# Kernel tuning notes

Measured on AMD Instinct MI355X. Metric: run time of the kernel, lower is better.

The kernel has to match this reference:

```python
import jax, jax.numpy as jnp
import numpy as np

N, E, M, NT, RB, SH, NIR, LAT = 10000, 160000, 8, 4, 8, 9, 3, 128
AVG_N = 16.0
LATF = LAT + M * NIR  # 152
COMP2IR = np.array([0, 1, 1, 1, 2, 2, 2, 2, 2])  # irrep id per SH component (0e,1o,2e)
IR1H = jnp.asarray(np.eye(NIR, dtype=np.float32)[COMP2IR])  # [9,3] one-hot comp->irrep


def _silu(x):
    return x * jax.nn.sigmoid(x)


def setup_inputs() -> dict:
    key = jax.random.key(0)
    ks = jax.random.split(key, 16)
    def w(k, shape, fan_in):
        return jax.random.normal(k, shape, jnp.float32) / np.sqrt(fan_in)
    return {
        'edge_attrs': jax.random.normal(ks[0], (E, SH), jnp.float32),
        'edge_embedding': jax.random.normal(ks[1], (E, RB), jnp.float32),
        'node_attrs': jax.random.uniform(ks[2], (N, NT), jnp.float32),
        'edge_lengths': jax.random.uniform(ks[3], (E,), jnp.float32),
        'tb_w0': w(ks[4], (2 * NT + RB, LAT), 2 * NT + RB),
        'tb_w1': w(ks[5], (LAT, LAT), LAT),
        'tb_w2': w(ks[6], (LAT, LAT), LAT),
        'env_mlp_w0': w(ks[7], (LAT, 2 * M * NIR), LAT),
        'env_mlp_w1': w(ks[8], (LAT, M * NIR), LAT),
        'env_linear_w': w(ks[9], (2, NIR, M, M), M),
        'latent_w': w(ks[10], (LATF, LAT), LATF),
        'lat2feat_w': w(ks[11], (2, LATF, NIR * M * M), LATF),
        'lat2featold_w': w(ks[12], (2, LATF, NIR * M * M), LATF),
        'final_w': w(ks[13], (LATF, M), LATF),
        'edge_index': jax.random.randint(ks[14], (2, E), 0, N, jnp.int32),
    }


def reference(edge_attrs, edge_embedding, node_attrs, edge_lengths,
              tb_w0, tb_w1, tb_w2, env_mlp_w0, env_mlp_w1, env_linear_w,
              latent_w, lat2feat_w, lat2featold_w, final_w, edge_index):
    center, neigh = edge_index[0], edge_index[1]
    n_nodes = node_attrs.shape[0]
    c2i = jnp.asarray(COMP2IR)

    # polynomial cutoff, p=6, x = r / r_max
    x = edge_lengths
    p = 6.0
    cut = (1.0 - (p + 1) * (p + 2) / 2 * x**6 + p * (p + 2) * x**7 - p * (p + 1) / 2 * x**8)
    cut = jnp.where(x < 1.0, cut, 0.0)[:, None]

    # two-body latent MLP on [center species, neighbor species, radial basis]
    tb_in = jnp.concatenate([node_attrs[center], node_attrs[neigh], edge_embedding], axis=-1)
    h = _silu(tb_in @ tb_w0)
    h = _silu(h @ tb_w1)
    latents = (h @ tb_w2) * cut  # [E, LAT]

    def weight_edges(wch):  # MakeWeightedChannels: per-irrep channel weights
        return wch[:, :, c2i] * edge_attrs[:, None, :]  # [E, M, 9]

    def env_of(w_cur, layer):  # scatter to node env + env linear
        env = jax.ops.segment_sum(weight_edges(w_cur), center, num_segments=n_nodes) / AVG_N
        Wc = env_linear_w[layer][c2i]  # [9, M, M]
        return jnp.einsum('duv,nvd->nud', Wc, env) / np.sqrt(M)

    def interact(features, env_c):  # scalar-gated equivariant coupling
        return features * env_c[:, :, :1] + env_c * features[:, :, :1]

    def invariants(f):  # per-(channel, irrep) norms
        return jnp.sqrt(jnp.einsum('eud,di->eui', f * f, IR1H) + 1e-8).reshape(f.shape[0], M * NIR)

    def pe_linear(Wflat, f):  # per-edge generated irrep-wise Linear
        W = Wflat.reshape(-1, NIR, M, M)
        return jnp.einsum('eiuv,di,evd->eud', W, IR1H, f) / np.sqrt(M)

    # ---- layer 0 (initial weighter + env weighter) ----
    ew = latents @ env_mlp_w0  # [E, 2*M*NIR]
    w_init = ew[:, :M * NIR].reshape(-1, M, NIR)
    w_cur = ew[:, M * NIR:].reshape(-1, M, NIR)
    features = weight_edges(w_init)  # [E, M, 9]
    env_c = env_of(w_cur, 0)[center]
    new_f = interact(features, env_c)
    lat_full = jnp.concatenate([latents, invariants(new_f)], axis=-1)  # [E, 152]
    features = 0.5 * pe_linear(lat_full @ lat2featold_w[0], features) \
             + 0.5 * pe_linear(lat_full @ lat2feat_w[0], new_f)

    # ---- layer 1 ----
    lat_new = _silu(lat_full @ latent_w) * cut
    latents = 0.5 * latents + 0.5 * lat_new  # latent resnet, sigmoid(0)=0.5
    w_cur = (latents @ env_mlp_w1).reshape(-1, M, NIR)
    env_c = env_of(w_cur, 1)[center]
    new_f = interact(features, env_c)
    lat_full = jnp.concatenate([latents, invariants(new_f)], axis=-1)
    features = 0.5 * pe_linear(lat_full @ lat2featold_w[1], features) \
             + 0.5 * pe_linear(lat_full @ lat2feat_w[1], new_f)

    # ---- final: generated linear to 1x1o per edge (components 1:4) ----
    wfin = lat_full @ final_w  # [E, M]
    return jnp.einsum('em,emd->ed', wfin, features[:, :, 1:4]) / np.sqrt(M)
```

## Files before the change

### kernel.cpp

```cpp
#include <hip/hip_runtime.h>
#include <hip/hip_bf16.h>

#define EE 160000
#define NNODES 10000

using bf16 = __hip_bfloat16;
using bf16x8 = __attribute__((ext_vector_type(8))) short;
using short4v = __attribute__((ext_vector_type(4))) short;
using f32x4  = __attribute__((ext_vector_type(4))) float;

__device__ __forceinline__ float silu_f(float x) { return x / (1.0f + __expf(-x)); }
__device__ __forceinline__ float b2f(bf16 v) { return __bfloat162float(v); }
__device__ __forceinline__ bf16 f2b(float v) { return __float2bfloat16(v); }

__device__ __forceinline__ unsigned bfbits(float v) {
    union { float f; unsigned u; } a; a.f = v;
    return (a.u + 0x7fffu + ((a.u >> 16) & 1u)) >> 16;
}
__device__ __forceinline__ unsigned pack2(float a, float b) {
    return bfbits(a) | (bfbits(b) << 16);
}
__device__ __forceinline__ void unpack2(unsigned u, float& a, float& b) {
    union { unsigned x; float f; } lo, hi;
    lo.x = u << 16; hi.x = u & 0xffff0000u;
    a = lo.f; b = hi.f;
}
__device__ __forceinline__ float bs2f(short s) {
    union { unsigned u; float f; } x; x.u = ((unsigned)(unsigned short)s) << 16;
    return x.f;
}

#define INV_AVGN_SQM 0.02209708691207961f
#define HALF_INV_SQM 0.17677669529663687f
#define INV_SQM      0.35355339059327373f

__global__ void kCnt(const int* __restrict__ eidx, int* __restrict__ deg)
{
    const int e = blockIdx.x * 256 + threadIdx.x;
    atomicAdd(&deg[eidx[e]], 1);
}

__global__ void kScan(const int* __restrict__ deg, int* __restrict__ off)
{
    __shared__ int part[256];
    const int t = threadIdx.x;
    int loc[40];
    int s = 0;
#pragma unroll
    for (int i = 0; i < 40; i++) {
        const int idx = t * 40 + i;
        const int v = (idx < NNODES) ? deg[idx] : 0;
        loc[i] = s;
        s += v;
    }
    part[t] = s;
    __syncthreads();
    for (int d = 1; d < 256; d <<= 1) {
        const int v = (t >= d) ? part[t - d] : 0;
        __syncthreads();
        part[t] += v;
        __syncthreads();
    }
    const int base = (t == 0) ? 0 : part[t - 1];
#pragma unroll
    for (int i = 0; i < 40; i++) {
        const int idx = t * 40 + i;
        if (idx < NNODES) off[idx] = base + loc[i];
    }
    if (t == 255) off[NNODES] = part[255];
}

__global__ void kFill(const int* __restrict__ eidx, int* __restrict__ cur,
                      const int* __restrict__ off, int* __restrict__ elist)
{
    const int e = blockIdx.x * 256 + threadIdx.x;
    const int c = eidx[e];
    const int pos = atomicAdd(&cur[c], 1);
    elist[off[c] + pos] = e;
}

__global__ void kPrepA(const float* __restrict__ w1, const float* __restrict__ w2,
                       const float* __restrict__ wm0, short* __restrict__ wAt)
{
    const int t = blockIdx.x * 256 + threadIdx.x;
    if (t >= 38912) return;
    const int k = t & 127, c = t >> 7;
    float v;
    if (c < 128)      v = w1[k * 128 + c];
    else if (c < 256) v = w2[k * 128 + (c - 128)];
    else              v = wm0[k * 48 + (c - 256)];
    wAt[c * 128 + k] = (short)bfbits(v);
}

__global__ void kPrepB(const float* __restrict__ l2fo, const float* __restrict__ l2fn,
                       const float* __restrict__ latw, const float* __restrict__ l2fo1,
                       const float* __restrict__ l2fn1, const float* __restrict__ finw,
                       const float* __restrict__ wm1, short* __restrict__ Bt)
{
    const int k = blockIdx.y;
    const int col = blockIdx.x * 256 + threadIdx.x;
    if (col >= 672) return;
    float v = 0.f;
    if (col < 648) {
        if (k < 152) {
            if (col < 384) {
                const int ir = col >> 7, half = (col >> 6) & 1, q = col & 63;
                const float* src = half ? l2fn : l2fo;
                v = src[k * 192 + ir * 64 + q];
            } else if (col < 512)  v = latw[k * 128 + (col - 384)];
            else if (col < 576)    v = l2fo1[k * 192 + 64 + (col - 512)];
            else if (col < 640)    v = l2fn1[k * 192 + 64 + (col - 576)];
            else                   v = finw[k * 8 + (col - 640)];
        }
    } else {
        if (k < 128) v = wm1[k * 24 + (col - 648)];
    }
    Bt[(size_t)col * 160 + k] = (short)bfbits(v);
}

__global__ void kEnvG(const float* __restrict__ wcur, const float* __restrict__ ea,
                      const int* __restrict__ off, const int* __restrict__ elist,
                      const float* __restrict__ wl, float* __restrict__ envc)
{
    const int t = blockIdx.x * 256 + threadIdx.x;
    if (t >= NNODES * 9) return;
    const int n = t / 9;
    const int d = t - n * 9;
    const int irr = (d == 0) ? 0 : ((d < 4) ? 1 : 2);
    float v[8];
#pragma unroll
    for (int q = 0; q < 8; q++) v[q] = 0.0f;
    const int b = off[n], en = off[n + 1];
    for (int j = b; j < en; j++) {
        const int e = elist[j];
        const float ad = ea[e * 9 + d];
        const float* wr = wcur + (size_t)e * 24 + irr;
#pragma unroll
        for (int q = 0; q < 8; q++) v[q] = fmaf(wr[q * 3], ad, v[q]);
    }
#pragma unroll
    for (int u = 0; u < 8; u++) {
        float s = 0.0f;
#pragma unroll
        for (int q = 0; q < 8; q++) s = fmaf(wl[irr * 64 + u * 8 + q], v[q], s);
        envc[n * 72 + u * 9 + d] = s * INV_AVGN_SQM;
    }
}

__global__ __launch_bounds__(256) void kA0(
    const float* __restrict__ ea, const float* __restrict__ eemb,
    const float* __restrict__ nat, const float* __restrict__ elen,
    const float* __restrict__ w0, const int* __restrict__ eidx,
    short* __restrict__ h08, short* __restrict__ latf8s,
    bf16* __restrict__ eaT, float* __restrict__ cutb)
{
    __shared__ float w0s[16 * 128];
    const int t = threadIdx.x;
    const int e = blockIdx.x * 256 + t;
#pragma unroll
    for (int p = 0; p < 8; p++) { const int idx = p * 256 + t; w0s[idx] = w0[idx]; }
    __syncthreads();

    const int ctr = eidx[e];
    const int ngb = eidx[EE + e];
    float tin[16];
#pragma unroll
    for (int k = 0; k < 4; k++) tin[k] = nat[ctr * 4 + k];
#pragma unroll
    for (int k = 0; k < 4; k++) tin[4 + k] = nat[ngb * 4 + k];
#pragma unroll
    for (int k = 0; k < 8; k++) tin[8 + k] = eemb[e * 8 + k];

    const float x = elen[e];
    const float x2 = x * x, x4 = x2 * x2, x6 = x4 * x2, x7 = x6 * x, x8 = x7 * x;
    float cutv = 1.0f - 28.0f * x6 + 48.0f * x7 - 21.0f * x8;
    cutv = (x < 1.0f) ? cutv : 0.0f;
    cutb[e] = cutv;

    const size_t tb = (size_t)(e >> 5);
    const int el = e & 31;
#pragma unroll
    for (int jc = 0; jc < 4; jc++) {
        float a[32];
#pragma unroll
        for (int j = 0; j < 32; j++) a[j] = 0.0f;
#pragma unroll
        for (int k = 0; k < 16; k++) {
            const float v = tin[k];
#pragma unroll
            for (int j = 0; j < 32; j++) a[j] = fmaf(v, w0s[k * 128 + jc * 32 + j], a[j]);
        }
#pragma unroll
        for (int cc = 0; cc < 4; cc++) {
            bf16x8 hv;
#pragma unroll
            for (int jj = 0; jj < 8; jj++) hv[jj] = (short)bfbits(silu_f(a[cc * 8 + jj]));
            *(bf16x8*)(h08 + tb * 4096 + (jc * 4 + cc) * 256 + el * 8) = hv;
        }
    }
    bf16x8 z;
#pragma unroll
    for (int jj = 0; jj < 8; jj++) z[jj] = 0;
    *(bf16x8*)(latf8s + tb * 5120 + 19 * 256 + el * 8) = z;

#pragma unroll
    for (int d = 0; d < 9; d++) eaT[(size_t)d * EE + e] = f2b(ea[e * 9 + d]);
}

__global__ __launch_bounds__(256, 2) void kAm(
    const short* __restrict__ h08, const short* __restrict__ wAt,
    const float* __restrict__ cutb, short* __restrict__ latf8s,
    float* __restrict__ winiF, float* __restrict__ wcur0)
{
    __shared__ short Bs[16 * 128 * 8];
    __shared__ alignas(16) char a2raw[16384];
    __shared__ short A3[8192];
    short* A2 = (short*)a2raw;
    float* Cs = (float*)a2raw;

    const int t = threadIdx.x;
    const int eb = blockIdx.x * 64;
    const int lane = t & 63, wid = t >> 6;
    const int wm = wid >> 1, wn = wid & 1;
    const int l15 = lane & 15, kq = lane >> 4;
    const f32x4 zz = {0.f, 0.f, 0.f, 0.f};

#pragma unroll
    for (int p = 0; p < 8; p++) {
        const int task = p * 256 + t;
        const int n = task & 127, kc = task >> 7;
        *(bf16x8*)(Bs + kc * 1024 + n * 8) = *(const bf16x8*)(wAt + n * 128 + kc * 8);
    }
    float cutR[2][4];
#pragma unroll
    for (int mi = 0; mi < 2; mi++)
#pragma unroll
        for (int r = 0; r < 4; r++)
            cutR[mi][r] = cutb[eb + wm * 32 + mi * 16 + kq * 4 + r];
    __syncthreads();

    {
        f32x4 acc[8];
#pragma unroll
        for (int q = 0; q < 8; q++) acc[q] = zz;
        const size_t ab = (size_t)((eb >> 5) + wm) * 4096 + l15 * 8;
#pragma unroll
        for (int ks = 0; ks < 4; ks++) {
            const int kc = ks * 4 + kq;
            const bf16x8 a0 = *(const bf16x8*)(h08 + ab + kc * 256);
            const bf16x8 a1 = *(const bf16x8*)(h08 + ab + kc * 256 + 128);
            const short* bp = Bs + kc * 1024 + (wn * 64 + l15) * 8;
#pragma unroll
            for (int ni = 0; ni < 4; ni++) {
                const bf16x8 b = *(const bf16x8*)(bp + ni * 128);
                acc[ni]     = __builtin_amdgcn_mfma_f32_16x16x32_bf16(a0, b, acc[ni], 0, 0, 0);
                acc[4 + ni] = __builtin_amdgcn_mfma_f32_16x16x32_bf16(a1, b, acc[4 + ni], 0, 0, 0);
            }
        }
#pragma unroll
        for (int mi = 0; mi < 2; mi++)
#pragma unroll
            for (int ni = 0; ni < 4; ni++) {
                const int kcol = wn * 64 + ni * 16 + l15;
                const int eb2 = wm * 32 + mi * 16 + (kq << 2);
#pragma unroll
                for (int r = 0; r < 4; r++)
                    A2[(kcol >> 3) * 512 + (eb2 + r) * 8 + (kcol & 7)] =
                        (short)bfbits(silu_f(acc[mi * 4 + ni][r]));
            }
    }
    __syncthreads();
#pragma unroll
    for (int p = 0; p < 8; p++) {
        const int task = p * 256 + t;
        const int n = task & 127, kc = task >> 7;
        *(bf16x8*)(Bs + kc * 1024 + n * 8) = *(const bf16x8*)(wAt + 16384 + n * 128 + kc * 8);
    }
    __syncthreads();

    {
        f32x4 acc[8];
#pragma unroll
        for (int q = 0; q < 8; q++) acc[q] = zz;
#pragma unroll
        for (int ks = 0; ks < 4; ks++) {
            const int kc = ks * 4 + kq;
            const bf16x8 a0 = *(const bf16x8*)(A2 + kc * 512 + (wm * 32 + l15) * 8);
            const bf16x8 a1 = *(const bf16x8*)(A2 + kc * 512 + (wm * 32 + 16 + l15) * 8);
            const short* bp = Bs + kc * 1024 + (wn * 64 + l15) * 8;
#pragma unroll
            for (int ni = 0; ni < 4; ni++) {
                const bf16x8 b = *(const bf16x8*)(bp + ni * 128);
                acc[ni]     = __builtin_amdgcn_mfma_f32_16x16x32_bf16(a0, b, acc[ni], 0, 0, 0);
                acc[4 + ni] = __builtin_amdgcn_mfma_f32_16x16x32_bf16(a1, b, acc[4 + ni], 0, 0, 0);
            }
        }
#pragma unroll
        for (int mi = 0; mi < 2; mi++)
#pragma unroll
            for (int ni = 0; ni < 4; ni++) {
                const int kcol = wn * 64 + ni * 16 + l15;
                const int eb2 = wm * 32 + mi * 16 + (kq << 2);
#pragma unroll
                for (int r = 0; r < 4; r++)
                    A3[(kcol >> 3) * 512 + (eb2 + r) * 8 + (kcol & 7)] =
                        (short)bfbits(acc[mi * 4 + ni][r] * cutR[mi][r]);
            }
    }
    __syncthreads();
#pragma unroll
    for (int p = 0; p < 8; p++) {
        const int task = p * 256 + t;
        const int n = task & 127, kc = task >> 7;
        bf16x8 bv;
        if (n < 48) bv = *(const bf16x8*)(wAt + 32768 + n * 128 + kc * 8);
        else {
#pragma unroll
            for (int jj = 0; jj < 8; jj++) bv[jj] = 0;
        }
        *(bf16x8*)(Bs + kc * 1024 + n * 8) = bv;
    }
#pragma unroll
    for (int p = 0; p < 4; p++) {
        const int i = p * 256 + t;
        const int e = i & 63, kc = i >> 6;
        const bf16x8 v = *(const bf16x8*)(A3 + kc * 512 + e * 8);
        const int eg = eb + e;
        *(bf16x8*)(latf8s + (size_t)(eg >> 5) * 5120 + kc * 256 + (eg & 31) * 8) = v;
    }
    __syncthreads();

    if (wn == 0) {
        f32x4 acc[6];
#pragma unroll
        for (int q = 0; q < 6; q++) acc[q] = zz;
#pragma unroll
        for (int ks = 0; ks < 4; ks++) {
            const int kc = ks * 4 + kq;
            const bf16x8 a0 = *(const bf16x8*)(A3 + kc * 512 + (wm * 32 + l15) * 8);
            const bf16x8 a1 = *(const bf16x8*)(A3 + kc * 512 + (wm * 32 + 16 + l15) * 8);
            const short* bp = Bs + kc * 1024 + l15 * 8;
#pragma unroll
            for (int ni = 0; ni < 3; ni++) {
                const bf16x8 b = *(const bf16x8*)(bp + ni * 128);
                acc[ni]     = __builtin_amdgcn_mfma_f32_16x16x32_bf16(a0, b, acc[ni], 0, 0, 0);
                acc[3 + ni] = __builtin_amdgcn_mfma_f32_16x16x32_bf16(a1, b, acc[3 + ni], 0, 0, 0);
            }
        }
#pragma unroll
        for (int mi = 0; mi < 2; mi++)
#pragma unroll
            for (int ni = 0; ni < 3; ni++) {
                const int c = ni * 16 + l15;
                const int eb2 = wm * 32 + mi * 16 + (kq << 2);
#pragma unroll
                for (int r = 0; r < 4; r++)
                    Cs[c * 65 + eb2 + r] = acc[mi * 3 + ni][r];
            }
    }
    __syncthreads();
    for (int i = t; i < 1536; i += 256) {
        const int c = i >> 6, e = i & 63;
        winiF[(size_t)c * EE + eb + e] = Cs[c * 65 + e];
    }
    for (int i = t; i < 1536; i += 256) {
        const int e2 = i / 24, c2 = i - e2 * 24;
        wcur0[(size_t)(eb + e2) * 24 + c2] = Cs[(24 + c2) * 65 + e2];
    }
}

__global__ __launch_bounds__(256, 1) void kC1(
    const float* __restrict__ winiF, const bf16* __restrict__ eaT,
    const float* __restrict__ envc, const int* __restrict__ eidx,
    unsigned* __restrict__ newfT, short* __restrict__ latf8s)
{
    const int e = blockIdx.x * 256 + threadIdx.x;
    const int ctr = eidx[e];
    float eav[9];
#pragma unroll
    for (int d = 0; d < 9; d++) eav[d] = b2f(eaT[(size_t)d * EE + e]);
    const float* ec = envc + ctr * 72;
    float inv[24];
#pragma unroll
    for (int uh = 0; uh < 4; uh++) {
        const int u0 = 2 * uh;
        float wi0[3], wi1[3];
#pragma unroll
        for (int i = 0; i < 3; i++) {
            wi0[i] = winiF[(size_t)(u0 * 3 + i) * EE + e];
            wi1[i] = winiF[(size_t)((u0 + 1) * 3 + i) * EE + e];
        }
        float nf0[9], nf1[9];
        const float ec00 = ec[u0 * 9 + 0];
        const float ec10 = ec[(u0 + 1) * 9 + 0];
        const float f00 = wi0[0] * eav[0];
        const float f10 = wi1[0] * eav[0];
#pragma unroll
        for (int d = 0; d < 9; d++) {
            const int irr = (d == 0) ? 0 : ((d < 4) ? 1 : 2);
            const float fa = wi0[irr] * eav[d];
            const float fb = wi1[irr] * eav[d];
            nf0[d] = fa * ec00 + ec[u0 * 9 + d] * f00;
            nf1[d] = fb * ec10 + ec[(u0 + 1) * 9 + d] * f10;
        }
#pragma unroll
        for (int d = 0; d < 9; d++) newfT[(size_t)(d * 4 + uh) * EE + e] = pack2(nf0[d], nf1[d]);
        inv[uh * 6 + 0] = sqrtf(nf0[0] * nf0[0] + 1e-8f);
        inv[uh * 6 + 1] = sqrtf(nf0[1]*nf0[1] + nf0[2]*nf0[2] + nf0[3]*nf0[3] + 1e-8f);
        inv[uh * 6 + 2] = sqrtf(nf0[4]*nf0[4] + nf0[5]*nf0[5] + nf0[6]*nf0[6] + nf0[7]*nf0[7] + nf0[8]*nf0[8] + 1e-8f);
        inv[uh * 6 + 3] = sqrtf(nf1[0] * nf1[0] + 1e-8f);
        inv[uh * 6 + 4] = sqrtf(nf1[1]*nf1[1] + nf1[2]*nf1[2] + nf1[3]*nf1[3] + 1e-8f);
        inv[uh * 6 + 5] = sqrtf(nf1[4]*nf1[4] + nf1[5]*nf1[5] + nf1[6]*nf1[6] + nf1[7]*nf1[7] + nf1[8]*nf1[8] + 1e-8f);
    }
    const size_t tb = (size_t)(e >> 5);
    const int el = e & 31;
#pragma unroll
    for (int j = 0; j < 3; j++) {
        bf16x8 iv;
#pragma unroll
        for (int jj = 0; jj < 8; jj++) iv[jj] = (short)bfbits(inv[j * 8 + jj]);
        *(bf16x8*)(latf8s + tb * 5120 + (16 + j) * 256 + el * 8) = iv;
    }
}

__global__ __launch_bounds__(256, 2) void kF0(
    const short* __restrict__ A8, const short* __restrict__ Bt,
    const float* __restrict__ winiF, const bf16* __restrict__ eaT,
    const unsigned* __restrict__ newfT, unsigned* __restrict__ feat1T)
{
    __shared__ short Bs[20480];
    __shared__ float Cs[128 * 67];
    const int t = threadIdx.x;
    const int eb = blockIdx.x * 64;
    const int lane = t & 63, wid = t >> 6;
    const int wm = wid >> 1, wn = wid & 1;
    const int l15 = lane & 15, kq = lane >> 4;
    const f32x4 zz = {0.f, 0.f, 0.f, 0.f};
    const size_t ab = (size_t)((eb >> 5) + wm) * 5120 + l15 * 8;
    const int te = t & 63, uh = t >> 6;
    const int eg = eb + te;

    for (int ir = 0; ir < 3; ir++) {
#pragma unroll
        for (int p = 0; p < 10; p++) {
            const int task = p * 256 + t;
            const int n = task & 127, kc = task >> 7;
            *(bf16x8*)(Bs + kc * 1024 + n * 8) =
                *(const bf16x8*)(Bt + (size_t)(ir * 128 + n) * 160 + kc * 8);
        }
        __syncthreads();
        f32x4 acc[8];
#pragma unroll
        for (int q = 0; q < 8; q++) acc[q] = zz;
#pragma unroll
        for (int ks = 0; ks < 5; ks++) {
            const int kc = ks * 4 + kq;
            const bf16x8 a0 = *(const bf16x8*)(A8 + ab + kc * 256);
            const bf16x8 a1 = *(const bf16x8*)(A8 + ab + kc * 256 + 128);
            const short* bp = Bs + kc * 1024 + (wn * 64 + l15) * 8;
#pragma unroll
            for (int ni = 0; ni < 4; ni++) {
                const bf16x8 b = *(const bf16x8*)(bp + ni * 128);
                acc[ni]     = __builtin_amdgcn_mfma_f32_16x16x32_bf16(a0, b, acc[ni], 0, 0, 0);
                acc[4 + ni] = __builtin_amdgcn_mfma_f32_16x16x32_bf16(a1, b, acc[4 + ni], 0, 0, 0);
            }
        }
#pragma unroll
        for (int mi = 0; mi < 2; mi++)
#pragma unroll
            for (int ni = 0; ni < 4; ni++) {
                const int cl = wn * 64 + ni * 16 + l15;
                const int el = wm * 32 + mi * 16 + (kq << 2);
                const f32x4 v = acc[mi * 4 + ni];
#pragma unroll
                for (int r = 0; r < 4; r++) Cs[cl * 67 + el + r] = v[r];
            }
        __syncthreads();
        const int d0 = (ir == 0) ? 0 : ((ir == 1) ? 1 : 4);
        const int nd = (ir == 0) ? 1 : ((ir == 1) ? 3 : 5);
        float wv[8];
#pragma unroll
        for (int v8 = 0; v8 < 8; v8++) wv[v8] = winiF[(size_t)(v8 * 3 + ir) * EE + eg];
        for (int dd = 0; dd < nd; dd++) {
            const int d = d0 + dd;
            const float ead = b2f(eaT[(size_t)d * EE + eg]);
            float nfv[8];
#pragma unroll
            for (int q = 0; q < 4; q++)
                unpack2(newfT[(size_t)(d * 4 + q) * EE + eg], nfv[2 * q], nfv[2 * q + 1]);
            float s0 = 0.f, s1 = 0.f;
#pragma unroll
            for (int v8 = 0; v8 < 8; v8++) {
                const float fe = wv[v8] * ead;
                s0 += Cs[(uh * 16 + v8) * 67 + te] * fe + Cs[(64 + uh * 16 + v8) * 67 + te] * nfv[v8];
                s1 += Cs[(uh * 16 + 8 + v8) * 67 + te] * fe + Cs[(64 + uh * 16 + 8 + v8) * 67 + te] * nfv[v8];
            }
            feat1T[(size_t)(d * 4 + uh) * EE + eg] = pack2(s0 * HALF_INV_SQM, s1 * HALF_INV_SQM);
        }
    }
}

__global__ __launch_bounds__(256, 2) void kF3(
    short* __restrict__ A8, const short* __restrict__ Bt,
    const float* __restrict__ cutb, float* __restrict__ wcur1)
{
    __shared__ short Bs[20480];
    __shared__ alignas(16) short Cc[128 * 68];
    __shared__ short l1s[16 * 512];
    float* Cw = (float*)Cc;
    const int t = threadIdx.x;
    const int eb = blockIdx.x * 64;
    const int lane = t & 63, wid = t >> 6;
    const int wm = wid >> 1, wn = wid & 1;
    const int l15 = lane & 15, kq = lane >> 4;
    const f32x4 zz = {0.f, 0.f, 0.f, 0.f};

#pragma unroll
    for (int p = 0; p < 10; p++) {
        const int task = p * 256 + t;
        const int n = task & 127, kc = task >> 7;
        *(bf16x8*)(Bs + kc * 1024 + n * 8) =
            *(const bf16x8*)(Bt + (size_t)(384 + n) * 160 + kc * 8);
    }
    __syncthreads();
    {
        f32x4 acc[8];
#pragma unroll
        for (int q = 0; q < 8; q++) acc[q] = zz;
        const size_t ab = (size_t)((eb >> 5) + wm) * 5120 + l15 * 8;
#pragma unroll
        for (int ks = 0; ks < 5; ks++) {
            const int kc = ks * 4 + kq;
            const bf16x8 a0 = *(const bf16x8*)(A8 + ab + kc * 256);
            const bf16x8 a1 = *(const bf16x8*)(A8 + ab + kc * 256 + 128);
            const short* bp = Bs + kc * 1024 + (wn * 64 + l15) * 8;
#pragma unroll
            for (int ni = 0; ni < 4; ni++) {
                const bf16x8 b = *(const bf16x8*)(bp + ni * 128);
                acc[ni]     = __builtin_amdgcn_mfma_f32_16x16x32_bf16(a0, b, acc[ni], 0, 0, 0);
                acc[4 + ni] = __builtin_amdgcn_mfma_f32_16x16x32_bf16(a1, b, acc[4 + ni], 0, 0, 0);
            }
        }
#pragma unroll
        for (int mi = 0; mi < 2; mi++)
#pragma unroll
            for (int ni = 0; ni < 4; ni++) {
                const int cl = wn * 64 + ni * 16 + l15;
                const int el = wm * 32 + mi * 16 + (kq << 2);
                const f32x4 v = acc[mi * 4 + ni];
                short4v pv;
#pragma unroll
                for (int r = 0; r < 4; r++) pv[r] = (short)bfbits(v[r]);
                *(short4v*)(Cc + cl * 68 + el) = pv;
            }
    }
    __syncthreads();
    {
        const int te = t & 63, q = t >> 6;
        const int eg = eb + te;
        const size_t tb = (size_t)(eg >> 5);
        const int el2 = eg & 31;
        const float cutv = cutb[eg];
#pragma unroll
        for (int c = 0; c < 4; c++) {
            const int kc = q * 4 + c;
            short* ap = A8 + tb * 5120 + kc * 256 + el2 * 8;
            const bf16x8 ov = *(const bf16x8*)ap;
            bf16x8 nv;
#pragma unroll
            for (int jj = 0; jj < 8; jj++) {
                const int j = kc * 8 + jj;
                const float g = bs2f(Cc[j * 68 + te]);
                const float o = bs2f(ov[jj]);
                nv[jj] = (short)bfbits(0.5f * o + 0.5f * silu_f(g) * cutv);
            }
            *(bf16x8*)ap = nv;
            *(bf16x8*)(l1s + kc * 512 + te * 8) = nv;
        }
    }
    for (int i = t; i < 384; i += 256) {
        const int n = i % 24, kc = i / 24;
        *(bf16x8*)(Bs + kc * 1024 + n * 8) =
            *(const bf16x8*)(Bt + (size_t)(648 + n) * 160 + kc * 8);
    }
    __syncthreads();
    if (wn == 0) {
        f32x4 acc[4] = {zz, zz, zz, zz};
#pragma unroll
        for (int ks = 0; ks < 4; ks++) {
            const int kc = ks * 4 + kq;
            const bf16x8 a0 = *(const bf16x8*)(l1s + kc * 512 + (wm * 32 + l15) * 8);
            const bf16x8 a1 = *(const bf16x8*)(l1s + kc * 512 + (wm * 32 + 16 + l15) * 8);
            const short* bp = Bs + kc * 1024 + l15 * 8;
#pragma unroll
            for (int ni = 0; ni < 2; ni++) {
                const bf16x8 b = *(const bf16x8*)(bp + ni * 128);
                acc[ni]     = __builtin_amdgcn_mfma_f32_16x16x32_bf16(a0, b, acc[ni], 0, 0, 0);
                acc[2 + ni] = __builtin_amdgcn_mfma_f32_16x16x32_bf16(a1, b, acc[2 + ni], 0, 0, 0);
            }
        }
#pragma unroll
        for (int mi = 0; mi < 2; mi++)
#pragma unroll
            for (int ni = 0; ni < 2; ni++) {
                const int c = ni * 16 + l15;
                if (c < 24) {
                    const int el = wm * 32 + mi * 16 + (kq << 2);
#pragma unroll
                    for (int r = 0; r < 4; r++) Cw[c * 65 + el + r] = acc[mi * 2 + ni][r];
                }
            }
    }
    __syncthreads();
    for (int i = t; i < 1536; i += 256) {
        const int e2 = i / 24, c2 = i - e2 * 24;
        wcur1[(size_t)(eb + e2) * 24 + c2] = Cw[c2 * 65 + e2];
    }
}

__global__ __launch_bounds__(256, 1) void kE1(
    const unsigned* __restrict__ feat1T, const float* __restrict__ envc,
    const int* __restrict__ eidx, unsigned* __restrict__ newfT,
    short* __restrict__ latf8s)
{
    const int e = blockIdx.x * 256 + threadIdx.x;
    const int ctr = eidx[e];
    const float* ec = envc + ctr * 72;
    float inv[24];
#pragma unroll
    for (int uh = 0; uh < 4; uh++) {
        const int u0 = 2 * uh;
        float f0[9], f1[9];
#pragma unroll
        for (int d = 0; d < 9; d++) unpack2(feat1T[(size_t)(d * 4 + uh) * EE + e], f0[d], f1[d]);
        const float ec00 = ec[u0 * 9 + 0];
        const float ec10 = ec[(u0 + 1) * 9 + 0];
        float nf0[9], nf1[9];
#pragma unroll
        for (int d = 0; d < 9; d++) {
            nf0[d] = f0[d] * ec00 + ec[u0 * 9 + d] * f0[0];
            nf1[d] = f1[d] * ec10 + ec[(u0 + 1) * 9 + d] * f1[0];
        }
#pragma unroll
        for (int d = 0; d < 9; d++) newfT[(size_t)(d * 4 + uh) * EE + e] = pack2(nf0[d], nf1[d]);
        inv[uh * 6 + 0] = sqrtf(nf0[0] * nf0[0] + 1e-8f);
        inv[uh * 6 + 1] = sqrtf(nf0[1]*nf0[1] + nf0[2]*nf0[2] + nf0[3]*nf0[3] + 1e-8f);
        inv[uh * 6 + 2] = sqrtf(nf0[4]*nf0[4] + nf0[5]*nf0[5] + nf0[6]*nf0[6] + nf0[7]*nf0[7] + nf0[8]*nf0[8] + 1e-8f);
        inv[uh * 6 + 3] = sqrtf(nf1[0] * nf1[0] + 1e-8f);
        inv[uh * 6 + 4] = sqrtf(nf1[1]*nf1[1] + nf1[2]*nf1[2] + nf1[3]*nf1[3] + 1e-8f);
        inv[uh * 6 + 5] = sqrtf(nf1[4]*nf1[4] + nf1[5]*nf1[5] + nf1[6]*nf1[6] + nf1[7]*nf1[7] + nf1[8]*nf1[8] + 1e-8f);
    }
    const size_t tb = (size_t)(e >> 5);
    const int el = e & 31;
#pragma unroll
    for (int j = 0; j < 3; j++) {
        bf16x8 iv;
#pragma unroll
        for (int jj = 0; jj < 8; jj++) iv[jj] = (short)bfbits(inv[j * 8 + jj]);
        *(bf16x8*)(latf8s + tb * 5120 + (16 + j) * 256 + el * 8) = iv;
    }
}

__global__ __launch_bounds__(256, 2) void kF2(
    const short* __restrict__ A8, const short* __restrict__ Bt,
    const unsigned* __restrict__ feat1T, const unsigned* __restrict__ newfT,
    float* __restrict__ outp)
{
    __shared__ short Bs[20480];
    __shared__ float Cs[128 * 67];
    __shared__ float Cwf[16 * 67];
    const int t = threadIdx.x;
    const int eb = blockIdx.x * 64;
    const int lane = t & 63, wid = t >> 6;
    const int wm = wid >> 1, wn = wid & 1;
    const int l15 = lane & 15, kq = lane >> 4;
    const f32x4 zz = {0.f, 0.f, 0.f, 0.f};
    const size_t ab = (size_t)((eb >> 5) + wm) * 5120 + l15 * 8;
#pragma unroll
    for (int p = 0; p < 10; p++) {
        const int task = p * 256 + t;
        const int n = task & 127, kc = task >> 7;
        *(bf16x8*)(Bs + kc * 1024 + n * 8) =
            *(const bf16x8*)(Bt + (size_t)(512 + n) * 160 + kc * 8);
    }
    __syncthreads();
    {
        f32x4 acc[8];
#pragma unroll
        for (int q = 0; q < 8; q++) acc[q] = zz;
#pragma unroll
        for (int ks = 0; ks < 5; ks++) {
            const int kc = ks * 4 + kq;
            const bf16x8 a0 = *(const bf16x8*)(A8 + ab + kc * 256);
            const bf16x8 a1 = *(const bf16x8*)(A8 + ab + kc * 256 + 128);
            const short* bp = Bs + kc * 1024 + (wn * 64 + l15) * 8;
#pragma unroll
            for (int ni = 0; ni < 4; ni++) {
                const bf16x8 b = *(const bf16x8*)(bp + ni * 128);
                acc[ni]     = __builtin_amdgcn_mfma_f32_16x16x32_bf16(a0, b, acc[ni], 0, 0, 0);
                acc[4 + ni] = __builtin_amdgcn_mfma_f32_16x16x32_bf16(a1, b, acc[4 + ni], 0, 0, 0);
            }
        }
#pragma unroll
        for (int mi = 0; mi < 2; mi++)
#pragma unroll
            for (int ni = 0; ni < 4; ni++) {
                const int cl = wn * 64 + ni * 16 + l15;
                const int el = wm * 32 + mi * 16 + (kq << 2);
                const f32x4 v = acc[mi * 4 + ni];
#pragma unroll
                for (int r = 0; r < 4; r++) Cs[cl * 67 + el + r] = v[r];
            }
    }
    __syncthreads();
    for (int i = t; i < 320; i += 256) {
        const int n = i & 15, kc = i >> 4;
        bf16x8 bv;
        if (n < 8) bv = *(const bf16x8*)(Bt + (size_t)(640 + n) * 160 + kc * 8);
        else {
#pragma unroll
            for (int jj = 0; jj < 8; jj++) bv[jj] = 0;
        }
        *(bf16x8*)(Bs + kc * 1024 + n * 8) = bv;
    }
    __syncthreads();
    {
        f32x4 a2[2] = {zz, zz};
#pragma unroll
        for (int ks = 0; ks < 5; ks++) {
            const int kc = ks * 4 + kq;
            const bf16x8 a0 = *(const bf16x8*)(A8 + ab + kc * 256);
            const bf16x8 a1 = *(const bf16x8*)(A8 + ab + kc * 256 + 128);
            const bf16x8 b = *(const bf16x8*)(Bs + kc * 1024 + l15 * 8);
            a2[0] = __builtin_amdgcn_mfma_f32_16x16x32_bf16(a0, b, a2[0], 0, 0, 0);
            a2[1] = __builtin_amdgcn_mfma_f32_16x16x32_bf16(a1, b, a2[1], 0, 0, 0);
        }
        if (wn == 0) {
#pragma unroll
            for (int mi = 0; mi < 2; mi++) {
                const int el = wm * 32 + mi * 16 + (kq << 2);
#pragma unroll
                for (int r = 0; r < 4; r++) Cwf[l15 * 67 + el + r] = a2[mi][r];
            }
        }
    }
    __syncthreads();
    if (t < 192) {
        const int te = t % 64;
        const int dd = t / 64;
        const int eg = eb + te;
        const int d = 1 + dd;
        float f1v[8], nfv[8];
#pragma unroll
        for (int q = 0; q < 4; q++) {
            unpack2(feat1T[(size_t)(d * 4 + q) * EE + eg], f1v[2 * q], f1v[2 * q + 1]);
            unpack2(newfT[(size_t)(d * 4 + q) * EE + eg], nfv[2 * q], nfv[2 * q + 1]);
        }
        float od = 0.f;
#pragma unroll
        for (int u = 0; u < 8; u++) {
            float s = 0.f;
#pragma unroll
            for (int v8 = 0; v8 < 8; v8++)
                s += Cs[(u * 8 + v8) * 67 + te] * f1v[v8] + Cs[(64 + u * 8 + v8) * 67 + te] * nfv[v8];
            od = fmaf(Cwf[u * 67 + te], s, od);
        }
        outp[(size_t)eg * 3 + dd] = od * (HALF_INV_SQM * INV_SQM);
    }
}

extern "C" void kernel_launch(void* const* d_in, const int* in_sizes, int n_in,
                              void* d_out, int out_size, void* d_ws, size_t ws_size,
                              hipStream_t stream)
{
    const float* ea   = (const float*)d_in[0];
    const float* eemb = (const float*)d_in[1];
    const float* nat  = (const float*)d_in[2];
    const float* elen = (const float*)d_in[3];
    const float* w0   = (const float*)d_in[4];
    const float* w1   = (const float*)d_in[5];
    const float* w2   = (const float*)d_in[6];
    const float* wm0  = (const float*)d_in[7];
    const float* wm1  = (const float*)d_in[8];
    const float* envl = (const float*)d_in[9];
    const float* latw = (const float*)d_in[10];
    const float* l2fn = (const float*)d_in[11];
    const float* l2fo = (const float*)d_in[12];
    const float* finw = (const float*)d_in[13];
    const int*   eidx = (const int*)d_in[14];

    char* ws = (char*)d_ws;
    short*    latf8s = (short*)(ws + 0);
    short*    h08    = (short*)(ws + 51200000);
    unsigned* newfT  = (unsigned*)(ws + 92160000);
    unsigned* feat1T = (unsigned*)(ws + 115200000);
    float*    winiF  = (float*)(ws + 138240000);
    bf16*     eaT    = (bf16*)(ws + 153600000);
    float*    cutb   = (float*)(ws + 156480000);
    float*    env0   = (float*)(ws + 157120000);
    float*    env1   = (float*)(ws + 160000000);
    int*      deg    = (int*)(ws + 162880000);
    int*      cur    = (int*)(ws + 162920000);
    int*      off    = (int*)(ws + 162960000);
    int*      elist  = (int*)(ws + 163000192);
    short*    wAt    = (short*)(ws + 162880000);
    short*    Bt     = (short*)(ws + 163640192);

    float* wcur0 = (float*)newfT;
    float* wcur1 = (float*)newfT;

    hipMemsetAsync(deg, 0, 80000, stream);

    kCnt <<<625, 256, 0, stream>>>(eidx, deg);
    kScan<<<1, 256, 0, stream>>>(deg, off);
    kFill<<<625, 256, 0, stream>>>(eidx, cur, off, elist);
    kPrepA<<<152, 256, 0, stream>>>(w1, w2, wm0, wAt);
    kPrepB<<<dim3(3, 160), 256, 0, stream>>>(l2fo, l2fn, latw,
                                             l2fo + 29184, l2fn + 29184, finw, wm1, Bt);

    kA0<<<625, 256, 0, stream>>>(ea, eemb, nat, elen, w0, eidx, h08, latf8s, eaT, cutb);
    kAm<<<2500, 256, 0, stream>>>(h08, wAt, cutb, latf8s, winiF, wcur0);
    kEnvG<<<352, 256, 0, stream>>>(wcur0, ea, off, elist, envl + 0, env0);
    kC1<<<625, 256, 0, stream>>>(winiF, eaT, env0, eidx, newfT, latf8s);

    kF0<<<2500, 256, 0, stream>>>(latf8s, Bt, winiF, eaT, newfT, feat1T);
    kF3<<<2500, 256, 0, stream>>>(latf8s, Bt, cutb, wcur1);
    kEnvG<<<352, 256, 0, stream>>>(wcur1, ea, off, elist, envl + 192, env1);
    kE1<<<625, 256, 0, stream>>>(feat1T, env1, eidx, newfT, latf8s);
    kF2<<<2500, 256, 0, stream>>>(latf8s, Bt, feat1T, newfT, (float*)d_out);
}
```

Before: 343.5 us.

## Read GEMM weight fragments directly from global memory instead of staging in LDS

Removes the shared-memory staging of the B (weight) matrices in kAm, kF0, kF3 and kF2. MFMA B fragments are now loaded straight from global memory, relying on L1/L2 caching of the small weight tensors. This drops several block-wide barriers and shrinks the LDS footprint, so launch bounds are raised from 2 to 4 blocks per CU. The cost is more global/L2 traffic per wave, with strided row accesses in place of LDS reads, and possibly more register pressure under the tighter occupancy bound.

```diff
diff --git a/kernel.cpp b/kernel.cpp
--- a/kernel.cpp
+++ b/kernel.cpp
@@ -207,12 +207,11 @@
     for (int d = 0; d < 9; d++) eaT[(size_t)d * EE + e] = f2b(ea[e * 9 + d]);
 }
 
-__global__ __launch_bounds__(256, 2) void kAm(
+__global__ __launch_bounds__(256, 4) void kAm(
     const short* __restrict__ h08, const short* __restrict__ wAt,
     const float* __restrict__ cutb, short* __restrict__ latf8s,
     float* __restrict__ winiF, float* __restrict__ wcur0)
 {
-    __shared__ short Bs[16 * 128 * 8];
     __shared__ alignas(16) char a2raw[16384];
     __shared__ short A3[8192];
     short* A2 = (short*)a2raw;
@@ -225,19 +224,12 @@
     const int l15 = lane & 15, kq = lane >> 4;
     const f32x4 zz = {0.f, 0.f, 0.f, 0.f};
 
-#pragma unroll
-    for (int p = 0; p < 8; p++) {
-        const int task = p * 256 + t;
-        const int n = task & 127, kc = task >> 7;
-        *(bf16x8*)(Bs + kc * 1024 + n * 8) = *(const bf16x8*)(wAt + n * 128 + kc * 8);
-    }
     float cutR[2][4];
 #pragma unroll
     for (int mi = 0; mi < 2; mi++)
 #pragma unroll
         for (int r = 0; r < 4; r++)
             cutR[mi][r] = cutb[eb + wm * 32 + mi * 16 + kq * 4 + r];
-    __syncthreads();
 
     {
         f32x4 acc[8];
@@ -249,10 +241,10 @@
             const int kc = ks * 4 + kq;
             const bf16x8 a0 = *(const bf16x8*)(h08 + ab + kc * 256);
             const bf16x8 a1 = *(const bf16x8*)(h08 + ab + kc * 256 + 128);
-            const short* bp = Bs + kc * 1024 + (wn * 64 + l15) * 8;
-#pragma unroll
-            for (int ni = 0; ni < 4; ni++) {
-                const bf16x8 b = *(const bf16x8*)(bp + ni * 128);
+            const short* bp = wAt + (wn * 64 + l15) * 128 + kc * 8;
+#pragma unroll
+            for (int ni = 0; ni < 4; ni++) {
+                const bf16x8 b = *(const bf16x8*)(bp + ni * 16 * 128);
                 acc[ni]     = __builtin_amdgcn_mfma_f32_16x16x32_bf16(a0, b, acc[ni], 0, 0, 0);
                 acc[4 + ni] = __builtin_amdgcn_mfma_f32_16x16x32_bf16(a1, b, acc[4 + ni], 0, 0, 0);
             }
@@ -268,13 +260,6 @@
                     A2[(kcol >> 3) * 512 + (eb2 + r) * 8 + (kcol & 7)] =
                         (short)bfbits(silu_f(acc[mi * 4 + ni][r]));
             }
-    }
-    __syncthreads();
-#pragma unroll
-    for (int p = 0; p < 8; p++) {
-        const int task = p * 256 + t;
-        const int n = task & 127, kc = task >> 7;
-        *(bf16x8*)(Bs + kc * 1024 + n * 8) = *(const bf16x8*)(wAt + 16384 + n * 128 + kc * 8);
     }
     __syncthreads();
 
@@ -287,10 +272,10 @@
             const int kc = ks * 4 + kq;
             const bf16x8 a0 = *(const bf16x8*)(A2 + kc * 512 + (wm * 32 + l15) * 8);
             const bf16x8 a1 = *(const bf16x8*)(A2 + kc * 512 + (wm * 32 + 16 + l15) * 8);
-            const short* bp = Bs + kc * 1024 + (wn * 64 + l15) * 8;
-#pragma unroll
-            for (int ni = 0; ni < 4; ni++) {
-                const bf16x8 b = *(const bf16x8*)(bp + ni * 128);
+            const short* bp = wAt + 16384 + (wn * 64 + l15) * 128 + kc * 8;
+#pragma unroll
+            for (int ni = 0; ni < 4; ni++) {
+                const bf16x8 b = *(const bf16x8*)(bp + ni * 16 * 128);
                 acc[ni]     = __builtin_amdgcn_mfma_f32_16x16x32_bf16(a0, b, acc[ni], 0, 0, 0);
                 acc[4 + ni] = __builtin_amdgcn_mfma_f32_16x16x32_bf16(a1, b, acc[4 + ni], 0, 0, 0);
             }
@@ -308,18 +293,6 @@
             }
     }
     __syncthreads();
-#pragma unroll
-    for (int p = 0; p < 8; p++) {
-        const int task = p * 256 + t;
-        const int n = task & 127, kc = task >> 7;
-        bf16x8 bv;
-        if (n < 48) bv = *(const bf16x8*)(wAt + 32768 + n * 128 + kc * 8);
-        else {
-#pragma unroll
-            for (int jj = 0; jj < 8; jj++) bv[jj] = 0;
-        }
-        *(bf16x8*)(Bs + kc * 1024 + n * 8) = bv;
-    }
 #pragma unroll
     for (int p = 0; p < 4; p++) {
         const int i = p * 256 + t;
@@ -328,7 +301,6 @@
         const int eg = eb + e;
         *(bf16x8*)(latf8s + (size_t)(eg >> 5) * 5120 + kc * 256 + (eg & 31) * 8) = v;
     }
-    __syncthreads();
 
     if (wn == 0) {
         f32x4 acc[6];
@@ -339,10 +311,10 @@
             const int kc = ks * 4 + kq;
             const bf16x8 a0 = *(const bf16x8*)(A3 + kc * 512 + (wm * 32 + l15) * 8);
             const bf16x8 a1 = *(const bf16x8*)(A3 + kc * 512 + (wm * 32 + 16 + l15) * 8);
-            const short* bp = Bs + kc * 1024 + l15 * 8;
+            const short* bp = wAt + 32768 + l15 * 128 + kc * 8;
 #pragma unroll
             for (int ni = 0; ni < 3; ni++) {
-                const bf16x8 b = *(const bf16x8*)(bp + ni * 128);
+                const bf16x8 b = *(const bf16x8*)(bp + ni * 16 * 128);
                 acc[ni]     = __builtin_amdgcn_mfma_f32_16x16x32_bf16(a0, b, acc[ni], 0, 0, 0);
                 acc[3 + ni] = __builtin_amdgcn_mfma_f32_16x16x32_bf16(a1, b, acc[3 + ni], 0, 0, 0);
             }
@@ -423,12 +395,11 @@
     }
 }
 
-__global__ __launch_bounds__(256, 2) void kF0(
+__global__ __launch_bounds__(256, 4) void kF0(
     const short* __restrict__ A8, const short* __restrict__ Bt,
     const float* __restrict__ winiF, const bf16* __restrict__ eaT,
     const unsigned* __restrict__ newfT, unsigned* __restrict__ feat1T)
 {
-    __shared__ short Bs[20480];
     __shared__ float Cs[128 * 67];
     const int t = threadIdx.x;
     const int eb = blockIdx.x * 64;
@@ -441,14 +412,6 @@
     const int eg = eb + te;
 
     for (int ir = 0; ir < 3; ir++) {
-#pragma unroll
-        for (int p = 0; p < 10; p++) {
-            const int task = p * 256 + t;
-            const int n = task & 127, kc = task >> 7;
-            *(bf16x8*)(Bs + kc * 1024 + n * 8) =
-                *(const bf16x8*)(Bt + (size_t)(ir * 128 + n) * 160 + kc * 8);
-        }
-        __syncthreads();
         f32x4 acc[8];
 #pragma unroll
         for (int q = 0; q < 8; q++) acc[q] = zz;
@@ -457,14 +420,15 @@
             const int kc = ks * 4 + kq;
             const bf16x8 a0 = *(const bf16x8*)(A8 + ab + kc * 256);
             const bf16x8 a1 = *(const bf16x8*)(A8 + ab + kc * 256 + 128);
-            const short* bp = Bs + kc * 1024 + (wn * 64 + l15) * 8;
-#pragma unroll
-            for (int ni = 0; ni < 4; ni++) {
-                const bf16x8 b = *(const bf16x8*)(bp + ni * 128);
+            const short* bp = Bt + (size_t)(ir * 128 + wn * 64 + l15) * 160 + kc * 8;
+#pragma unroll
+            for (int ni = 0; ni < 4; ni++) {
+                const bf16x8 b = *(const bf16x8*)(bp + (size_t)ni * 16 * 160);
                 acc[ni]     = __builtin_amdgcn_mfma_f32_16x16x32_bf16(a0, b, acc[ni], 0, 0, 0);
                 acc[4 + ni] = __builtin_amdgcn_mfma_f32_16x16x32_bf16(a1, b, acc[4 + ni], 0, 0, 0);
             }
         }
+        __syncthreads();
 #pragma unroll
         for (int mi = 0; mi < 2; mi++)
 #pragma unroll
@@ -500,11 +464,10 @@
     }
 }
 
-__global__ __launch_bounds__(256, 2) void kF3(
+__global__ __launch_bounds__(256, 4) void kF3(
     short* __restrict__ A8, const short* __restrict__ Bt,
     const float* __restrict__ cutb, float* __restrict__ wcur1)
 {
-    __shared__ short Bs[20480];
     __shared__ alignas(16) short Cc[128 * 68];
     __shared__ short l1s[16 * 512];
     float* Cw = (float*)Cc;
@@ -515,14 +478,6 @@
     const int l15 = lane & 15, kq = lane >> 4;
     const f32x4 zz = {0.f, 0.f, 0.f, 0.f};
 
-#pragma unroll
-    for (int p = 0; p < 10; p++) {
-        const int task = p * 256 + t;
-        const int n = task & 127, kc = task >> 7;
-        *(bf16x8*)(Bs + kc * 1024 + n * 8) =
-            *(const bf16x8*)(Bt + (size_t)(384 + n) * 160 + kc * 8);
-    }
-    __syncthreads();
     {
         f32x4 acc[8];
 #pragma unroll
@@ -533,10 +488,10 @@
             const int kc = ks * 4 + kq;
             const bf16x8 a0 = *(const bf16x8*)(A8 + ab + kc * 256);
             const bf16x8 a1 = *(const bf16x8*)(A8 + ab + kc * 256 + 128);
-            const short* bp = Bs + kc * 1024 + (wn * 64 + l15) * 8;
-#pragma unroll
-            for (int ni = 0; ni < 4; ni++) {
-                const bf16x8 b = *(const bf16x8*)(bp + ni * 128);
+            const short* bp = Bt + (size_t)(384 + wn * 64 + l15) * 160 + kc * 8;
+#pragma unroll
+            for (int ni = 0; ni < 4; ni++) {
+                const bf16x8 b = *(const bf16x8*)(bp + (size_t)ni * 16 * 160);
                 acc[ni]     = __builtin_amdgcn_mfma_f32_16x16x32_bf16(a0, b, acc[ni], 0, 0, 0);
                 acc[4 + ni] = __builtin_amdgcn_mfma_f32_16x16x32_bf16(a1, b, acc[4 + ni], 0, 0, 0);
             }
@@ -578,11 +533,6 @@
             *(bf16x8*)(l1s + kc * 512 + te * 8) = nv;
         }
     }
-    for (int i = t; i < 384; i += 256) {
-        const int n = i % 24, kc = i / 24;
-        *(bf16x8*)(Bs + kc * 1024 + n * 8) =
-            *(const bf16x8*)(Bt + (size_t)(648 + n) * 160 + kc * 8);
-    }
     __syncthreads();
     if (wn == 0) {
         f32x4 acc[4] = {zz, zz, zz, zz};
@@ -591,10 +541,15 @@
             const int kc = ks * 4 + kq;
             const bf16x8 a0 = *(const bf16x8*)(l1s + kc * 512 + (wm * 32 + l15) * 8);
             const bf16x8 a1 = *(const bf16x8*)(l1s + kc * 512 + (wm * 32 + 16 + l15) * 8);
-            const short* bp = Bs + kc * 1024 + l15 * 8;
 #pragma unroll
             for (int ni = 0; ni < 2; ni++) {
-                const bf16x8 b = *(const bf16x8*)(bp + ni * 128);
+                const int c = ni * 16 + l15;
+                bf16x8 b;
+                if (c < 24) b = *(const bf16x8*)(Bt + (size_t)(648 + c) * 160 + kc * 8);
+                else {
+#pragma unroll
+                    for (int jj = 0; jj < 8; jj++) b[jj] = 0;
+                }
                 acc[ni]     = __builtin_amdgcn_mfma_f32_16x16x32_bf16(a0, b, acc[ni], 0, 0, 0);
                 acc[2 + ni] = __builtin_amdgcn_mfma_f32_16x16x32_bf16(a1, b, acc[2 + ni], 0, 0, 0);
             }
@@ -661,12 +616,11 @@
     }
 }
 
-__global__ __launch_bounds__(256, 2) void kF2(
+__global__ __launch_bounds__(256, 4) void kF2(
     const short* __restrict__ A8, const short* __restrict__ Bt,
     const unsigned* __restrict__ feat1T, const unsigned* __restrict__ newfT,
     float* __restrict__ outp)
 {
-    __shared__ short Bs[20480];
     __shared__ float Cs[128 * 67];
     __shared__ float Cwf[16 * 67];
     const int t = threadIdx.x;
@@ -676,14 +630,7 @@
     const int l15 = lane & 15, kq = lane >> 4;
     const f32x4 zz = {0.f, 0.f, 0.f, 0.f};
     const size_t ab = (size_t)((eb >> 5) + wm) * 5120 + l15 * 8;
-#pragma unroll
-    for (int p = 0; p < 10; p++) {
-        const int task = p * 256 + t;
-        const int n = task & 127, kc = task >> 7;
-        *(bf16x8*)(Bs + kc * 1024 + n * 8) =
-            *(const bf16x8*)(Bt + (size_t)(512 + n) * 160 + kc * 8);
-    }
-    __syncthreads();
+
     {
         f32x4 acc[8];
 #pragma unroll
@@ -693,10 +640,10 @@
             const int kc = ks * 4 + kq;
             const bf16x8 a0 = *(const bf16x8*)(A8 + ab + kc * 256);
             const bf16x8 a1 = *(const bf16x8*)(A8 + ab + kc * 256 + 128);
-            const short* bp = Bs + kc * 1024 + (wn * 64 + l15) * 8;
-#pragma unroll
-            for (int ni = 0; ni < 4; ni++) {
-                const bf16x8 b = *(const bf16x8*)(bp + ni * 128);
+            const short* bp = Bt + (size_t)(512 + wn * 64 + l15) * 160 + kc * 8;
+#pragma unroll
+            for (int ni = 0; ni < 4; ni++) {
+                const bf16x8 b = *(const bf16x8*)(bp + (size_t)ni * 16 * 160);
                 acc[ni]     = __builtin_amdgcn_mfma_f32_16x16x32_bf16(a0, b, acc[ni], 0, 0, 0);
                 acc[4 + ni] = __builtin_amdgcn_mfma_f32_16x16x32_bf16(a1, b, acc[4 + ni], 0, 0, 0);
             }
@@ -712,26 +659,18 @@
                 for (int r = 0; r < 4; r++) Cs[cl * 67 + el + r] = v[r];
             }
     }
-    __syncthreads();
-    for (int i = t; i < 320; i += 256) {
-        const int n = i & 15, kc = i >> 4;
-        bf16x8 bv;
-        if (n < 8) bv = *(const bf16x8*)(Bt + (size_t)(640 + n) * 160 + kc * 8);
-        else {
-#pragma unroll
-            for (int jj = 0; jj < 8; jj++) bv[jj] = 0;
-        }
-        *(bf16x8*)(Bs + kc * 1024 + n * 8) = bv;
-    }
-    __syncthreads();
     {
         f32x4 a2[2] = {zz, zz};
+        bf16x8 bz;
+#pragma unroll
+        for (int jj = 0; jj < 8; jj++) bz[jj] = 0;
 #pragma unroll
         for (int ks = 0; ks < 5; ks++) {
             const int kc = ks * 4 + kq;
             const bf16x8 a0 = *(const bf16x8*)(A8 + ab + kc * 256);
             const bf16x8 a1 = *(const bf16x8*)(A8 + ab + kc * 256 + 128);
-            const bf16x8 b = *(const bf16x8*)(Bs + kc * 1024 + l15 * 8);
+            const bf16x8 b = (l15 < 8)
+                ? *(const bf16x8*)(Bt + (size_t)(640 + l15) * 160 + kc * 8) : bz;
             a2[0] = __builtin_amdgcn_mfma_f32_16x16x32_bf16(a0, b, a2[0], 0, 0, 0);
             a2[1] = __builtin_amdgcn_mfma_f32_16x16x32_bf16(a1, b, a2[1], 0, 0, 0);
         }
```

Measured after the change: 366.9 us. +6.8%, slower.
